# Optimization experiments

Hardware: AMD Instinct MI355X
Metric: run time of the kernel (lower is better)

Reference implementation:

```python
import jax, jax.numpy as jnp
import numpy as np

B = 1_048_576
W = 64  # hidden width
N_FREQ = 6   # 3 dims * 6 freqs * (sin,cos) = 36
K_BLOB = 4   # one-blob bins per dim


def _freq_embed(p):
    # [B,3] -> [B,36]
    freqs = 2.0 ** jnp.arange(N_FREQ, dtype=p.dtype)
    ang = jnp.pi * p[:, :, None] * freqs  # [B,3,6]
    return jnp.concatenate([jnp.sin(ang), jnp.cos(ang)], axis=-1).reshape(p.shape[0], 3 * 2 * N_FREQ)


def _sph(d):
    # unit-square parameterization of a direction, [B,3] -> [B,2]
    d = d / (jnp.linalg.norm(d, axis=-1, keepdims=True) + 1e-8)
    u = jnp.arctan2(d[:, 1], d[:, 0]) / (2.0 * jnp.pi) + 0.5
    v = jnp.arccos(jnp.clip(d[:, 2], -1.0 + 1e-6, 1.0 - 1e-6)) / jnp.pi
    return jnp.stack([u, v], axis=-1)


def _one_blob(x, k=K_BLOB):
    # x in [0,1], [B,D] -> [B,D*k] Gaussian one-blob encoding
    centers = (jnp.arange(k, dtype=x.dtype) + 0.5) / k
    sigma = 1.0 / k
    g = jnp.exp(-0.5 * ((x[..., None] - centers) / sigma) ** 2)  # [B,D,k]
    return g.reshape(x.shape[0], -1)


def _encode(p, wi, n, alpha, beta, r):
    ones = jnp.ones((p.shape[0], 2), dtype=p.dtype)
    return jnp.concatenate([
        _freq_embed(p),                      # 36
        _one_blob(_sph(wi)),                 # 8
        _one_blob(_sph(n)),                  # 8
        _one_blob(1.0 - jnp.exp(-r)),        # 4
        alpha, beta,                         # 6
        ones,                                # 2 (implicit bias)
    ], axis=-1)                              # -> [B,64]


def _mlp(x, Ws):
    h = x
    for Wk in Ws[:-1]:
        h = jax.nn.relu(h @ Wk.T)
    return h @ Ws[-1].T  # [B,3]


def setup_inputs() -> dict:
    key = jax.random.key(0)
    ks = jax.random.split(key, 13)
    p = jax.random.normal(ks[0], (B, 3), jnp.float32)
    wi = jax.random.normal(ks[1], (B, 3), jnp.float32)
    n = jax.random.normal(ks[2], (B, 3), jnp.float32)
    alpha = jax.random.uniform(ks[3], (B, 3), jnp.float32)
    beta = jax.random.uniform(ks[4], (B, 3), jnp.float32)
    r = jax.random.uniform(ks[5], (B, 1), jnp.float32)
    s = 1.0 / np.sqrt(W)
    weights = {}
    for i in range(6):
        weights[f"W{i}"] = jax.random.normal(ks[6 + i], (W, W), jnp.float32) * s
    weights["W6"] = jax.random.normal(ks[12], (3, W), jnp.float32) * s
    return dict(p=p, wi=wi, n=n, alpha=alpha, beta=beta, r=r, **weights)


def reference(p, wi, n, alpha, beta, r, W0, W1, W2, W3, W4, W5, W6):
    x = _encode(p, wi, n, alpha, beta, r)
    out = _mlp(x, [W0, W1, W2, W3, W4, W5, W6])
    return out * (alpha + beta)  # reflectance factorization
```

## Files before the change

kernel.cpp:

```cpp
#include <hip/hip_runtime.h>


typedef _Float16 f16;
typedef f16 f16x2 __attribute__((ext_vector_type(2)));
typedef f16 f16x4 __attribute__((ext_vector_type(4)));
typedef f16 f16x8 __attribute__((ext_vector_type(8)));
typedef float f32x4 __attribute__((ext_vector_type(4)));

#define MFMA16(A, B, C) __builtin_amdgcn_mfma_f32_16x16x16f16(A, B, C, 0, 0, 0)
#define LDS_FENCE() __asm__ volatile("" ::: "memory")

static constexpr int TILES = 4;
static constexpr int BLOCK = 64;
static constexpr int SPB   = 64;

static constexpr int    WUNITS   = 50;
static constexpr size_t WS_BYTES = (size_t)WUNITS * 64 * 16;

__device__ __forceinline__ f16x2 pkh(float a, float b) {
    return __builtin_bit_cast(f16x2, __builtin_amdgcn_cvt_pkrtz(a, b));
}

__device__ __forceinline__ f16x8 pack8(const float* f) {
    f16x2 a = pkh(f[0], f[1]);
    f16x2 b = pkh(f[2], f[3]);
    f16x2 c = pkh(f[4], f[5]);
    f16x2 d = pkh(f[6], f[7]);
    f16x8 v;
    v[0] = a[0]; v[1] = a[1]; v[2] = b[0]; v[3] = b[1];
    v[4] = c[0]; v[5] = c[1]; v[6] = d[0]; v[7] = d[1];
    return v;
}

__device__ __forceinline__ f16x4 pack4(f32x4 v) {
    f16x2 a = pkh(v[0], v[1]);
    f16x2 b = pkh(v[2], v[3]);
    f16x4 r;
    r[0] = a[0]; r[1] = a[1]; r[2] = b[0]; r[3] = b[1];
    return r;
}

__device__ __forceinline__ float fast_atan2_rev(float y, float x) {
    const float ax = __builtin_fabsf(x), ay = __builtin_fabsf(y);
    const float mx = fmaxf(ax, ay), mn = fminf(ax, ay);
    const float a = mn * __builtin_amdgcn_rcpf(fmaxf(mx, 1e-30f));
    const float s = a * a;
    float r = a * (0.99997726f + s * (-0.33262347f + s * (0.19354346f +
              s * (-0.11643287f + s * (0.05265332f - s * 0.01172120f)))));
    if (ay > ax) r = 1.5707963268f - r;
    if (x < 0.0f) r = 3.1415926536f - r;
    r = (y < 0.0f) ? -r : r;
    return r * 0.15915494309189535f;
}

__device__ __forceinline__ float fast_acos(float x) {
    const float ax = __builtin_fabsf(x);
    const float t = __builtin_amdgcn_sqrtf(1.0f - ax);
    const float p = t * (1.5707288f + ax * (-0.2121144f +
                    ax * (0.0742610f - ax * 0.0187293f)));
    return (x < 0.0f) ? (3.1415926536f - p) : p;
}

__device__ __forceinline__ void blob4(float x, float* out) {
    const float dx = x - 0.125f;
    const float E0 = __expf(-8.0f * dx * dx);
    const float R  = __expf(4.0f * dx);
    const float t1 = R * 0.60653066f;
    const float t2 = R * 0.22313016f;
    const float t3 = R * 0.082084999f;
    out[0] = E0;
    out[1] = E0 * t1;
    out[2] = out[1] * t2;
    out[3] = out[2] * t3;
}

__global__ __launch_bounds__(256, 1) void pack_weights_kernel(
    const float* __restrict__ W0, const float* __restrict__ W1,
    const float* __restrict__ W2, const float* __restrict__ W3,
    const float* __restrict__ W4, const float* __restrict__ W5,
    const float* __restrict__ W6, f16* __restrict__ ws)
{
    const int u = (int)blockIdx.x * 256 + threadIdx.x;
    if (u >= WUNITS * 64) return;
    const int lane = u & 63;
    const int unit = u >> 6;
    const int q = lane >> 4, m = lane & 15;
    f16x8 v;
    if (unit < 48) {
        const int l = unit >> 3, rem = unit & 7;
        const int mt = rem >> 1, kbh = rem & 1;
        const float* Ws[6] = {W0, W1, W2, W3, W4, W5};
        const float* __restrict__ Wl = Ws[l];
#pragma unroll
        for (int e = 0; e < 8; ++e) {
            const int kb = kbh * 2 + (e >> 2), j = e & 3;
            v[e] = (f16)Wl[(mt * 16 + m) * 64 + kb * 16 + q * 4 + j];
        }
    } else {
        const int kbh = unit - 48;
#pragma unroll
        for (int e = 0; e < 8; ++e) {
            const int kb = kbh * 2 + (e >> 2), j = e & 3;
            v[e] = (m < 3) ? (f16)W6[m * 64 + kb * 16 + q * 4 + j] : (f16)0.0f;
        }
    }
    *(f16x8*)(ws + unit * 512 + lane * 8) = v;
}

__device__ __forceinline__ f16x4 lo4(f16x8 v) {
    return __builtin_shufflevector(v, v, 0, 1, 2, 3);
}
__device__ __forceinline__ f16x4 hi4(f16x8 v) {
    return __builtin_shufflevector(v, v, 4, 5, 6, 7);
}

template<int PACKED>
__global__ __launch_bounds__(BLOCK, 3) void nrc_mlp_kernel(
    const float* __restrict__ P,  const float* __restrict__ WI,
    const float* __restrict__ NV, const float* __restrict__ AL,
    const float* __restrict__ BE, const float* __restrict__ RR,
    const f16*   __restrict__ ws,
    const float* __restrict__ W0, const float* __restrict__ W1,
    const float* __restrict__ W2, const float* __restrict__ W3,
    const float* __restrict__ W4, const float* __restrict__ W5,
    const float* __restrict__ W6, float* __restrict__ Out)
{
    __shared__ __attribute__((aligned(16))) unsigned char smem[TILES * 2048 + TILES * 16 * 16];

    const int lane = threadIdx.x & 63;
    const int q    = lane >> 4;
    const int m    = lane & 15;
    unsigned char* const hb  = smem;
    unsigned char* const abb = smem + TILES * 2048;

    const int wave_base = (int)blockIdx.x * SPB;

    {
        const int s = wave_base + lane;

        float pv[3], wv[3], nv[3], av[3], bv[3];
#pragma unroll
        for (int d = 0; d < 3; ++d) {
            pv[d] = P [s * 3 + d];
            wv[d] = WI[s * 3 + d];
            nv[d] = NV[s * 3 + d];
            av[d] = AL[s * 3 + d];
            bv[d] = BE[s * 3 + d];
        }
        const float rv = RR[s];

        float feat[64];
#pragma unroll
        for (int d = 0; d < 3; ++d) {
            const float fr = __builtin_amdgcn_fractf(pv[d] * 0.5f);
            float sv = __builtin_amdgcn_sinf(fr);
            float cv = __builtin_amdgcn_cosf(fr);
            feat[d * 12 + 0] = sv;
            feat[d * 12 + 6] = cv;
#pragma unroll
            for (int k = 1; k < 6; ++k) {
                const float s2 = sv * sv;
                const float sc = sv * cv;
                cv = fmaf(-2.0f, s2, 1.0f);
                sv = sc + sc;
                feat[d * 12 + k]     = sv;
                feat[d * 12 + 6 + k] = cv;
            }
        }
#pragma unroll
        for (int which = 0; which < 2; ++which) {
            const float* dv = (which == 0) ? wv : nv;
            const int fo = 36 + which * 8;
            const float nr = __builtin_amdgcn_sqrtf(dv[0]*dv[0] + dv[1]*dv[1] + dv[2]*dv[2]) + 1e-8f;
            const float u  = fast_atan2_rev(dv[1], dv[0]) + 0.5f;
            float zc = dv[2] * __builtin_amdgcn_rcpf(nr);
            zc = fminf(fmaxf(zc, -1.0f + 1e-6f), 1.0f - 1e-6f);
            const float vv = fast_acos(zc) * 0.3183098861837907f;
            blob4(u,  &feat[fo]);
            blob4(vv, &feat[fo + 4]);
        }
        blob4(1.0f - __expf(-rv), &feat[52]);

        feat[56] = av[0]; feat[57] = av[1]; feat[58] = av[2];
        feat[59] = bv[0]; feat[60] = bv[1]; feat[61] = bv[2];
        feat[62] = 1.0f;  feat[63] = 1.0f;

        f32x4 abv;
        abv[0] = av[0] + bv[0]; abv[1] = av[1] + bv[1];
        abv[2] = av[2] + bv[2]; abv[3] = 0.0f;
        *(f32x4*)(abb + lane * 16) = abv;

        const int te = lane >> 4, me = lane & 15;
        unsigned char* const tb = hb + te * 2048 + me * 128;
#pragma unroll
        for (int g = 0; g < 8; ++g) {
            const int slot0 = (4 * g + 4 * me) & 31;
            *(f16x8*)(tb + slot0 * 4) = pack8(&feat[g * 8]);
        }
    }
    LDS_FENCE();

    f16x4 bf[TILES][4];
#pragma unroll
    for (int t = 0; t < TILES; ++t) {
#pragma unroll
        for (int kb = 0; kb < 4; ++kb) {
            const int s0 = (kb * 8 + q * 2 + 4 * m) & 31;
            bf[t][kb] = *(const f16x4*)(hb + t * 2048 + m * 128 + s0 * 4);
        }
    }

    const f16* const wbase = ws + (size_t)lane * 8;
    const float* const Ws[6] = {W0, W1, W2, W3, W4, W5};
    const f16x4 zero4 = {(f16)0.0f, (f16)0.0f, (f16)0.0f, (f16)0.0f};

#pragma unroll
    for (int layer = 0; layer < 6; ++layer) {
        f16x4 wa[4][4];
        if (PACKED) {
#pragma unroll
            for (int i = 0; i < 8; ++i) {
                const f16x8 v = *(const f16x8*)(wbase + (layer * 8 + i) * 512);
                const int mt = i >> 1, kbh = i & 1;
                wa[mt][kbh * 2]     = lo4(v);
                wa[mt][kbh * 2 + 1] = hi4(v);
            }
        } else {
            const float* __restrict__ Wl = Ws[layer];
#pragma unroll
            for (int mt = 0; mt < 4; ++mt)
#pragma unroll
                for (int kb = 0; kb < 4; ++kb)
                    wa[mt][kb] = pack4(*(const f32x4*)(Wl + (mt * 16 + m) * 64 + kb * 16 + q * 4));
        }

#pragma unroll
        for (int t = 0; t < TILES; ++t) {
            f32x4 acc[4];
#pragma unroll
            for (int mt = 0; mt < 4; ++mt) {
                f32x4 z = {0.0f, 0.0f, 0.0f, 0.0f};
#pragma unroll
                for (int kb = 0; kb < 4; ++kb)
                    z = MFMA16(wa[mt][kb], bf[t][kb], z);
                acc[mt] = z;
            }
#pragma unroll
            for (int mt = 0; mt < 4; ++mt)
                bf[t][mt] = __builtin_elementwise_max(pack4(acc[mt]), zero4);
        }
    }

    {
        f16x4 w6a[4];
        if (PACKED) {
            const f16x8 v0 = *(const f16x8*)(wbase + 48 * 512);
            const f16x8 v1 = *(const f16x8*)(wbase + 49 * 512);
            w6a[0] = lo4(v0); w6a[1] = hi4(v0);
            w6a[2] = lo4(v1); w6a[3] = hi4(v1);
        } else {
#pragma unroll
            for (int kb = 0; kb < 4; ++kb) {
                f32x4 t4 = {0.0f, 0.0f, 0.0f, 0.0f};
                if (m < 3) t4 = *(const f32x4*)(W6 + m * 64 + kb * 16 + q * 4);
                w6a[kb] = pack4(t4);
            }
        }
#pragma unroll
        for (int t = 0; t < TILES; ++t) {
            f32x4 z = {0.0f, 0.0f, 0.0f, 0.0f};
#pragma unroll
            for (int kb = 0; kb < 4; ++kb)
                z = MFMA16(w6a[kb], bf[t][kb], z);
            const f32x4 abv = *(const f32x4*)(abb + (t * 16 + m) * 16);
            if (lane < 16) {
                const int s = wave_base + t * 16 + m;
                float* o = Out + s * 3;
                o[0] = z[0] * abv[0];
                o[1] = z[1] * abv[1];
                o[2] = z[2] * abv[2];
            }
        }
    }
}

extern "C" void kernel_launch(void* const* d_in, const int* in_sizes, int n_in,
                              void* d_out, int out_size, void* d_ws, size_t ws_size,
                              hipStream_t stream) {
    (void)n_in; (void)out_size;
    const float* P  = (const float*)d_in[0];
    const float* WI = (const float*)d_in[1];
    const float* NV = (const float*)d_in[2];
    const float* AL = (const float*)d_in[3];
    const float* BE = (const float*)d_in[4];
    const float* RR = (const float*)d_in[5];
    const float* W0 = (const float*)d_in[6];
    const float* W1 = (const float*)d_in[7];
    const float* W2 = (const float*)d_in[8];
    const float* W3 = (const float*)d_in[9];
    const float* W4 = (const float*)d_in[10];
    const float* W5 = (const float*)d_in[11];
    const float* W6 = (const float*)d_in[12];
    f16*   ws  = (f16*)d_ws;
    float* Out = (float*)d_out;

    const int Bn = in_sizes[0] / 3;
    const int grid = Bn / SPB;

    if (ws_size >= WS_BYTES) {
        hipLaunchKernelGGL(pack_weights_kernel, dim3((WUNITS * 64 + 255) / 256),
                           dim3(256), 0, stream, W0, W1, W2, W3, W4, W5, W6, ws);
        hipLaunchKernelGGL((nrc_mlp_kernel<1>), dim3(grid), dim3(BLOCK), 0, stream,
                           P, WI, NV, AL, BE, RR, ws,
                           W0, W1, W2, W3, W4, W5, W6, Out);
    } else {
        hipLaunchKernelGGL((nrc_mlp_kernel<0>), dim3(grid), dim3(BLOCK), 0, stream,
                           P, WI, NV, AL, BE, RR, ws,
                           W0, W1, W2, W3, W4, W5, W6, Out);
    }
}
```

Baseline: 169.3 us.

## Switch to 16x16x32 f16 MFMA with permuted weight layout, two waves per block

Replaces the 16x16x16 MFMA chain with the gfx950 16x16x32 f16 instruction, halving the MFMA count per tile. The hidden activations stay in registers in the output fragment order, and the weight K columns are permuted (tau) when packed so they match that order without any shuffles. Blocks now hold two waves with separate LDS regions, and launch bounds go from 3 to 4. The permuted packing is easy to get wrong, and the larger blocks change occupancy.

```diff
diff --git a/kernel.cpp b/kernel.cpp
--- a/kernel.cpp
+++ b/kernel.cpp
@@ -7,15 +7,20 @@
 typedef f16 f16x8 __attribute__((ext_vector_type(8)));
 typedef float f32x4 __attribute__((ext_vector_type(4)));
 
-#define MFMA16(A, B, C) __builtin_amdgcn_mfma_f32_16x16x16f16(A, B, C, 0, 0, 0)
+#define MFMA32(A, B, C) __builtin_amdgcn_mfma_f32_16x16x32_f16(A, B, C, 0, 0, 0)
 #define LDS_FENCE() __asm__ volatile("" ::: "memory")
 
 static constexpr int TILES = 4;
-static constexpr int BLOCK = 64;
-static constexpr int SPB   = 64;
+static constexpr int WAVES = 2;
+static constexpr int BLOCK = WAVES * 64;
+static constexpr int SPB   = WAVES * 64;
 
 static constexpr int    WUNITS   = 50;
 static constexpr size_t WS_BYTES = (size_t)WUNITS * 64 * 16;
+
+__host__ __device__ __forceinline__ int tau(int x) {
+    return (x & 32) + ((x & 7) >> 2) * 16 + ((x >> 3) & 3) * 4 + (x & 3);
+}
 
 __device__ __forceinline__ f16x2 pkh(float a, float b) {
     return __builtin_bit_cast(f16x2, __builtin_amdgcn_cvt_pkrtz(a, b));
@@ -87,35 +92,32 @@
     const int q = lane >> 4, m = lane & 15;
     f16x8 v;
     if (unit < 48) {
-        const int l = unit >> 3, rem = unit & 7;
-        const int mt = rem >> 1, kbh = rem & 1;
+        const int l = unit >> 3, kt = (unit & 7) >> 2, mt = unit & 3;
         const float* Ws[6] = {W0, W1, W2, W3, W4, W5};
         const float* __restrict__ Wl = Ws[l];
 #pragma unroll
-        for (int e = 0; e < 8; ++e) {
-            const int kb = kbh * 2 + (e >> 2), j = e & 3;
-            v[e] = (f16)Wl[(mt * 16 + m) * 64 + kb * 16 + q * 4 + j];
+        for (int j = 0; j < 8; ++j) {
+            const int x = kt * 32 + q * 8 + j;
+            const int src = (l == 0) ? x : tau(x);
+            v[j] = (f16)Wl[(mt * 16 + m) * 64 + src];
         }
     } else {
-        const int kbh = unit - 48;
-#pragma unroll
-        for (int e = 0; e < 8; ++e) {
-            const int kb = kbh * 2 + (e >> 2), j = e & 3;
-            v[e] = (m < 3) ? (f16)W6[m * 64 + kb * 16 + q * 4 + j] : (f16)0.0f;
+        const int kt = unit - 48;
+#pragma unroll
+        for (int j = 0; j < 8; ++j) {
+            const int src = tau(kt * 32 + q * 8 + j);
+            v[j] = (m < 3) ? (f16)W6[m * 64 + src] : (f16)0.0f;
         }
     }
     *(f16x8*)(ws + unit * 512 + lane * 8) = v;
 }
 
-__device__ __forceinline__ f16x4 lo4(f16x8 v) {
-    return __builtin_shufflevector(v, v, 0, 1, 2, 3);
-}
-__device__ __forceinline__ f16x4 hi4(f16x8 v) {
-    return __builtin_shufflevector(v, v, 4, 5, 6, 7);
+__device__ __forceinline__ f16x8 cat44(f16x4 a, f16x4 b) {
+    return __builtin_shufflevector(a, b, 0, 1, 2, 3, 4, 5, 6, 7);
 }
 
 template<int PACKED>
-__global__ __launch_bounds__(BLOCK, 3) void nrc_mlp_kernel(
+__global__ __launch_bounds__(BLOCK, 4) void nrc_mlp_kernel(
     const float* __restrict__ P,  const float* __restrict__ WI,
     const float* __restrict__ NV, const float* __restrict__ AL,
     const float* __restrict__ BE, const float* __restrict__ RR,
@@ -125,15 +127,17 @@
     const float* __restrict__ W4, const float* __restrict__ W5,
     const float* __restrict__ W6, float* __restrict__ Out)
 {
-    __shared__ __attribute__((aligned(16))) unsigned char smem[TILES * 2048 + TILES * 16 * 16];
-
-    const int lane = threadIdx.x & 63;
+    __shared__ __attribute__((aligned(16))) unsigned char smem[WAVES * 9216];
+
+    const int tid  = threadIdx.x;
+    const int lane = tid & 63;
+    const int w    = tid >> 6;
     const int q    = lane >> 4;
     const int m    = lane & 15;
-    unsigned char* const hb  = smem;
-    unsigned char* const abb = smem + TILES * 2048;
-
-    const int wave_base = (int)blockIdx.x * SPB;
+    unsigned char* const hb  = smem + w * 9216;
+    unsigned char* const abb = hb + 8192;
+
+    const int wave_base = (int)blockIdx.x * SPB + w * 64;
 
     {
         const int s = wave_base + lane;
@@ -200,13 +204,13 @@
     }
     LDS_FENCE();
 
-    f16x4 bf[TILES][4];
+    f16x8 bf[TILES][2];
 #pragma unroll
     for (int t = 0; t < TILES; ++t) {
 #pragma unroll
-        for (int kb = 0; kb < 4; ++kb) {
-            const int s0 = (kb * 8 + q * 2 + 4 * m) & 31;
-            bf[t][kb] = *(const f16x4*)(hb + t * 2048 + m * 128 + s0 * 4);
+        for (int kt = 0; kt < 2; ++kt) {
+            const int s0 = (16 * kt + 4 * q + 4 * m) & 31;
+            bf[t][kt] = *(const f16x8*)(hb + t * 2048 + m * 128 + s0 * 4);
         }
     }
 
@@ -216,22 +220,25 @@
 
 #pragma unroll
     for (int layer = 0; layer < 6; ++layer) {
-        f16x4 wa[4][4];
+        f16x8 wa[8];
         if (PACKED) {
 #pragma unroll
-            for (int i = 0; i < 8; ++i) {
-                const f16x8 v = *(const f16x8*)(wbase + (layer * 8 + i) * 512);
-                const int mt = i >> 1, kbh = i & 1;
-                wa[mt][kbh * 2]     = lo4(v);
-                wa[mt][kbh * 2 + 1] = hi4(v);
-            }
+            for (int f = 0; f < 8; ++f)
+                wa[f] = *(const f16x8*)(wbase + (layer * 8 + f) * 512);
         } else {
             const float* __restrict__ Wl = Ws[layer];
 #pragma unroll
-            for (int mt = 0; mt < 4; ++mt)
-#pragma unroll
-                for (int kb = 0; kb < 4; ++kb)
-                    wa[mt][kb] = pack4(*(const f32x4*)(Wl + (mt * 16 + m) * 64 + kb * 16 + q * 4));
+            for (int kt = 0; kt < 2; ++kt)
+#pragma unroll
+                for (int mt = 0; mt < 4; ++mt) {
+                    float tv[8];
+#pragma unroll
+                    for (int j = 0; j < 8; ++j) {
+                        const int x = kt * 32 + q * 8 + j;
+                        tv[j] = Wl[(mt * 16 + m) * 64 + (layer == 0 ? x : tau(x))];
+                    }
+                    wa[kt * 4 + mt] = pack8(tv);
+                }
         }
 
 #pragma unroll
@@ -240,38 +247,41 @@
 #pragma unroll
             for (int mt = 0; mt < 4; ++mt) {
                 f32x4 z = {0.0f, 0.0f, 0.0f, 0.0f};
-#pragma unroll
-                for (int kb = 0; kb < 4; ++kb)
-                    z = MFMA16(wa[mt][kb], bf[t][kb], z);
+                z = MFMA32(wa[mt],     bf[t][0], z);
+                z = MFMA32(wa[4 + mt], bf[t][1], z);
                 acc[mt] = z;
             }
+            f16x4 pk[4];
 #pragma unroll
             for (int mt = 0; mt < 4; ++mt)
-                bf[t][mt] = __builtin_elementwise_max(pack4(acc[mt]), zero4);
+                pk[mt] = __builtin_elementwise_max(pack4(acc[mt]), zero4);
+            bf[t][0] = cat44(pk[0], pk[1]);
+            bf[t][1] = cat44(pk[2], pk[3]);
         }
     }
 
     {
-        f16x4 w6a[4];
+        f16x8 w6f[2];
         if (PACKED) {
-            const f16x8 v0 = *(const f16x8*)(wbase + 48 * 512);
-            const f16x8 v1 = *(const f16x8*)(wbase + 49 * 512);
-            w6a[0] = lo4(v0); w6a[1] = hi4(v0);
-            w6a[2] = lo4(v1); w6a[3] = hi4(v1);
+            w6f[0] = *(const f16x8*)(wbase + 48 * 512);
+            w6f[1] = *(const f16x8*)(wbase + 49 * 512);
         } else {
 #pragma unroll
-            for (int kb = 0; kb < 4; ++kb) {
-                f32x4 t4 = {0.0f, 0.0f, 0.0f, 0.0f};
-                if (m < 3) t4 = *(const f32x4*)(W6 + m * 64 + kb * 16 + q * 4);
-                w6a[kb] = pack4(t4);
+            for (int kt = 0; kt < 2; ++kt) {
+                float tv[8];
+#pragma unroll
+                for (int j = 0; j < 8; ++j) {
+                    const int src = tau(kt * 32 + q * 8 + j);
+                    tv[j] = (m < 3) ? W6[m * 64 + src] : 0.0f;
+                }
+                w6f[kt] = pack8(tv);
             }
         }
 #pragma unroll
         for (int t = 0; t < TILES; ++t) {
             f32x4 z = {0.0f, 0.0f, 0.0f, 0.0f};
-#pragma unroll
-            for (int kb = 0; kb < 4; ++kb)
-                z = MFMA16(w6a[kb], bf[t][kb], z);
+            z = MFMA32(w6f[0], bf[t][0], z);
+            z = MFMA32(w6f[1], bf[t][1], z);
             const f32x4 abv = *(const f32x4*)(abb + (t * 16 + m) * 16);
             if (lane < 16) {
                 const int s = wave_base + t * 16 + m;
```

After: 163.8 us. 1.03x faster.
